# Performance work log

Measured on AMD Instinct MI355X. Metric: run time of the kernel, lower is better.

The kernel has to match this reference:

```python
import jax, jax.numpy as jnp
import numpy as np

WL = 140        # window_length
TD_NUM = 14     # TimeDelayEnd - TimeDelaySta = 21 - 7
OFC = 119       # window_length - TimeDelayEnd
E1 = 119        # td_attn embed dim
E2 = 16         # cm_attn embed dim


def _mha(q, k, v, in_w, in_b, out_w, out_b):
    # single-head MultiheadAttention, torch convention: y = x @ W.T + b
    E = q.shape[-1]
    qp = q @ in_w[:E].T + in_b[:E]
    kp = k @ in_w[E:2 * E].T + in_b[E:2 * E]
    vp = v @ in_w[2 * E:].T + in_b[2 * E:]
    attn = jax.nn.softmax((qp * (E ** -0.5)) @ kp.T, axis=-1)
    return (attn @ vp) @ out_w.T + out_b


def setup_inputs() -> dict:
    key = jax.random.key(0)
    ks = jax.random.split(key, 24)
    n = lambda i, s: jax.random.normal(ks[i], s, dtype=jnp.float32) * 0.05
    return {
        "x": jax.random.normal(ks[0], (1, 1, 18, WL), dtype=jnp.float32),
        "td_in_w": n(1, (3 * E1, E1)), "td_in_b": n(2, (3 * E1,)),
        "td_out_w": n(3, (E1, E1)), "td_out_b": n(4, (E1,)),
        "cm_in_w": n(5, (4, 3 * E2, E2)), "cm_in_b": n(6, (4, 3 * E2)),
        "cm_out_w": n(7, (4, E2, E2)), "cm_out_b": n(8, (4, E2)),
        "mc_w": n(9, (2, 16)), "mc_b": n(10, (2,)),
        "max_fc_w": n(11, (16, 32)), "max_fc_b": n(12, (16,)),
        "proj_w": n(13, (2, 16)),
        "ln_g": jnp.ones((16,), jnp.float32), "ln_b": jnp.zeros((16,), jnp.float32),
        "fc_w": n(14, (2,)), "fc_b": n(15, (2,)),
        "out1_w": n(16, (OFC, 2 * OFC)), "out1_b": n(17, (OFC,)),
        "out2_w": n(18, (2, OFC)), "out2_b": n(19, (2,)),
    }


def reference(x, td_in_w, td_in_b, td_out_w, td_out_b,
              cm_in_w, cm_in_b, cm_out_w, cm_out_b,
              mc_w, mc_b, max_fc_w, max_fc_b, proj_w,
              ln_g, ln_b, fc_w, fc_b, out1_w, out1_b, out2_w, out2_b):
    wavA = x[0, 0, 0]            # [140]
    eeg = x[0, 0, 1:17]          # [16, 140]
    wavB = x[0, 0, 17]           # [140]

    # ChannelWav: vectorized sliding-window gather -> [OFC, TD_NUM]
    idx = jnp.arange(OFC)[:, None] + jnp.arange(TD_NUM)[None, :]
    wA_win = wavA[idx]           # [119, 14]
    wB_win = wavB[idx]

    eeg_q = eeg[:, WL - OFC:]    # [16, 119] (16 eeg channels as seq, embed=119)

    # time-delay attention: query=eeg (len 16), key/value=delayed wav (len 14)
    wA_att = _mha(eeg_q, wA_win.T, wA_win.T, td_in_w, td_in_b, td_out_w, td_out_b)  # [16,119]
    wB_att = _mha(eeg_q, wB_win.T, wB_win.T, td_in_w, td_in_b, td_out_w, td_out_b)

    # select_max: bmm + 1x1 conv + relu + fc + argmax over 16 scores
    vA = jax.nn.relu(mc_w[0] @ (eeg_q @ wA_att.T) + mc_b[0])   # [16]
    vB = jax.nn.relu(mc_w[1] @ (eeg_q @ wB_att.T) + mc_b[1])
    weight = jax.nn.relu(max_fc_w @ jnp.concatenate([vA, vB]) + max_fc_b)
    mi = jnp.argmax(weight)     # note: clamped into [0, TD_NUM) by jnp.take
    wA_sel = jnp.take(wA_win.T, mi, axis=0)   # [119]
    wB_sel = jnp.take(wB_win.T, mi, axis=0)

    # proj_audio: Conv1d(1,16,1,bias=False) == outer product with weight vector
    wA_p = proj_w[0][:, None] * wA_sel[None, :]   # [16,119]
    wB_p = proj_w[1][:, None] * wB_sel[None, :]

    # LayerNorm over the 16-channel axis
    et = eeg_q.T                                   # [119,16]
    mu = et.mean(-1, keepdims=True)
    var = et.var(-1, keepdims=True)
    eeg_ln = (((et - mu) / jnp.sqrt(var + 1e-5)) * ln_g + ln_b).T   # [16,119]

    data = [wA_p, eeg_ln, eeg_ln, wB_p]
    kv = [eeg_ln, wA_p, wB_p, eeg_ln]
    outs = [_mha(data[i].T, kv[i].T, kv[i].T,
                 cm_in_w[i], cm_in_b[i], cm_out_w[i], cm_out_b[i]).T
            for i in range(4)]                      # each [16,119]

    # tensordot + diag == per-position channel dot product
    d0 = jnp.einsum('ct,ct->t', outs[0], outs[1])   # [119]
    d1 = jnp.einsum('ct,ct->t', outs[3], outs[2])
    s0 = jax.nn.sigmoid(fc_w[0] * d0 + fc_b[0])
    s1 = jax.nn.sigmoid(fc_w[1] * d1 + fc_b[1])
    dd = jnp.concatenate([s0, s1])                  # [238]

    h = jax.nn.sigmoid(out1_w @ dd + out1_b)
    return jax.nn.sigmoid(out2_w @ h + out2_b)[None, :]   # [1,2]
```

## Files before the change

### kernel.cpp

```cpp
#include <hip/hip_runtime.h>
#include <math.h>


#define NWG 8
#define NT  1024

constexpr int WLEN = 140;
constexpr int TDN  = 14;
constexpr int NOFC = 119;

constexpr int G_V16 = 0;
constexpr int G_DD  = 64;

constexpr int EEG = 0;
constexpr int WA  = 1904;
constexpr int WB  = 2044;
constexpr int LNT = 2184;
constexpr int QP4 = 4088;
constexpr int Z4  = 4564;
constexpr int UD  = 5040;
constexpr int WTT = 5160;
constexpr int WVV = 5280;
constexpr int VT  = 5400;
constexpr int SC4 = 5416;
constexpr int BKQ = 5472;
constexpr int CVB = 5476, CBO = 5477;
constexpr int WQH = 5480;
constexpr int WKL = 5496;
constexpr int WVL = 5512;
constexpr int WQT = 5528;
constexpr int CST = 5544;
constexpr int AC  = 5548;
constexpr int BC  = 5564;
constexpr int G1L = 5580;
constexpr int MXT = 5612;
constexpr int MXB = 6124;
constexpr int WK2 = 6852;
constexpr int C2K = 6868;
constexpr int CQK = 6884;
constexpr int CBK = 6885;
constexpr int VPS = 8756;
constexpr int S1H = 11136;
constexpr int S2H = 11255;
constexpr int OWS = 11376;
constexpr int OBS = 11632;
constexpr int O1W = 11648;
constexpr int O1B = 15248;
constexpr int O2WS= 15264;
constexpr int O2B = 15294;
constexpr int FCW = 15296;
constexpr int FCB = 15298;
constexpr int DDL = 15300;
constexpr int HHL = 15538;
constexpr int VSL = 15554;
constexpr int ARENA = 15586;

struct Args {
  const float *x, *td_in_w, *td_in_b, *td_out_w, *td_out_b;
  const float *cm_in_w, *cm_in_b, *cm_out_w, *cm_out_b;
  const float *mc_w, *mc_b, *max_fc_w, *max_fc_b, *proj_w;
  const float *ln_g, *ln_b, *fc_w, *fc_b;
  const float *out1_w, *out1_b, *out2_w, *out2_b;
  float *out;
  unsigned int *bar;
  float *G;
};

__device__ __forceinline__ float sigmf(float v) {
  return 1.0f / (1.0f + __expf(-v));
}

__device__ __forceinline__ void gbar(unsigned int* p) {
  __syncthreads();
  if (threadIdx.x == 0) {
    __hip_atomic_fetch_add(p, 1u, __ATOMIC_ACQ_REL, __HIP_MEMORY_SCOPE_AGENT);
    while (__hip_atomic_load(p, __ATOMIC_RELAXED, __HIP_MEMORY_SCOPE_AGENT) < (unsigned)NWG) {
      __builtin_amdgcn_s_sleep(1);
    }
    __builtin_amdgcn_fence(__ATOMIC_ACQUIRE, "agent");
  }
  __syncthreads();
}

__device__ __forceinline__ float dot119(const float* __restrict__ w,
                                        const float* __restrict__ x,
                                        int lane16) {
  float a0 = 0.f, a1 = 0.f;
#pragma unroll
  for (int t = 0; t < 7; ++t) {
    float wv = w[lane16 + 16 * t];
    float xv = x[lane16 + 16 * t];
    if (t & 1) a1 += wv * xv; else a0 += wv * xv;
  }
  if (lane16 < 7) a0 += w[112 + lane16] * x[112 + lane16];
  float acc = a0 + a1;
#pragma unroll
  for (int m = 1; m < 16; m <<= 1) acc += __shfl_xor(acc, m);
  return acc;
}

__device__ __forceinline__ float dot16f4(const float* __restrict__ x,
                                         const float* __restrict__ w) {
  const float4* xa = (const float4*)x; const float4* wa = (const float4*)w;
  float4 x0 = xa[0], x1 = xa[1], x2 = xa[2], x3 = xa[3];
  float4 w0 = wa[0], w1 = wa[1], w2 = wa[2], w3 = wa[3];
  float d0 = x0.x*w0.x + x0.y*w0.y + x0.z*w0.z + x0.w*w0.w;
  float d1 = x1.x*w1.x + x1.y*w1.y + x1.z*w1.z + x1.w*w1.w;
  float d2 = x2.x*w2.x + x2.y*w2.y + x2.z*w2.z + x2.w*w2.w;
  float d3 = x3.x*w3.x + x3.y*w3.y + x3.z*w3.z + x3.w*w3.w;
  return (d0 + d1) + (d2 + d3);
}

__global__ __launch_bounds__(NT) void fused_cnn_kernel(Args a) {
  __shared__ __align__(16) float S[ARENA];
  const int tid = threadIdx.x;
  const int wgid = blockIdx.x;
  const int grp = tid >> 4;
  const int lane16 = tid & 15;
  float* G = a.G;

  const int s  = wgid >> 2;
  const int i0 = (wgid & 3) * 4;
  const int mh = s ? 3 : 0;
  const int lm = s ? 2 : 1;
  const int q4 = wgid & 3;
  const int r0 = q4 * 30;
  const int nr = (q4 == 3) ? 29 : 30;
  const int wavX = s ? WB : WA;

  for (int t = tid; t < 16 * NOFC; t += NT) {
    int c = t / NOFC, tt = t - c * NOFC;
    S[EEG + t] = a.x[(1 + c) * WLEN + (WLEN - NOFC) + tt];
  }
  if (tid < WLEN) {
    S[WA + tid] = a.x[tid];
    S[WB + tid] = a.x[17 * WLEN + tid];
  }
  if (tid < 512) {
    int t16 = tid >> 5, c32 = tid & 31;
    S[MXT + c32 * 16 + t16] = a.max_fc_w[tid];
  }
  if (tid < 16)  S[MXB + tid] = a.max_fc_b[tid];
  if (tid < 256) {
    int c = tid >> 4, e = tid & 15;
    S[OWS + e * 16 + c] = a.cm_out_w[mh * 256 + tid];
  }
  if (tid < 16)  S[OBS + tid] = a.cm_out_b[mh * 16 + tid];
  for (int idx = tid; idx < 15 * 238; idx += NT) {
    int rl = idx / 238, c = idx - rl * 238;
    int r = wgid * 15 + rl;
    S[O1W + rl * 240 + c] = (r < NOFC) ? a.out1_w[r * 238 + c] : 0.0f;
  }
  if (tid < 15) {
    int r = wgid * 15 + tid;
    S[O1B + tid] = (r < NOFC) ? a.out1_b[r] : 0.0f;
  }
  if (tid < 30) {
    int o = tid / 15, j = tid - o * 15;
    int r = wgid * 15 + j;
    S[O2WS + tid] = (r < NOFC) ? a.out2_w[o * NOFC + r] : 0.0f;
  }
  if (tid < 2) {
    S[O2B + tid] = a.out2_b[tid];
    S[FCW + tid] = a.fc_w[tid];
    S[FCB + tid] = a.fc_b[tid];
  }
  __syncthreads();

  for (int e = grp; e < NOFC; e += 64) {
    const float* wrow = a.td_in_w + e * NOFC;
    float w0 = wrow[lane16], w1 = wrow[lane16 + 16], w2 = wrow[lane16 + 32],
          w3 = wrow[lane16 + 48], w4 = wrow[lane16 + 64], w5 = wrow[lane16 + 80],
          w6 = wrow[lane16 + 96];
    float wt7 = (lane16 < 7) ? wrow[112 + lane16] : 0.0f;
    float b = a.td_in_b[e];
#pragma unroll
    for (int kk = 0; kk < 4; ++kk) {
      const float* x = S + EEG + (i0 + kk) * NOFC;
      float acc = w0 * x[lane16] + w1 * x[lane16 + 16] + w2 * x[lane16 + 32]
                + w3 * x[lane16 + 48] + w4 * x[lane16 + 64] + w5 * x[lane16 + 80]
                + w6 * x[lane16 + 96];
      if (lane16 < 7) acc += wt7 * x[112 + lane16];
#pragma unroll
      for (int mm = 1; mm < 16; mm <<= 1) acc += __shfl_xor(acc, mm);
      if (lane16 == 0) S[QP4 + kk * NOFC + e] = acc + b;
    }
  }
  if (grp >= 55) {
    int d = (grp - 55) * 16 + lane16;
    if (d < NOFC) {
      float acc = 0.f;
#pragma unroll
      for (int i = 0; i < 16; ++i) acc += a.mc_w[s * 16 + i] * S[EEG + i * NOFC + d];
      S[UD + d] = acc;
    }
  }
  __syncthreads();

  if (tid < NOFC) {
    float a0 = 0.f, a1 = 0.f, a2 = 0.f, a3 = 0.f;
    const float* base = a.td_in_w + NOFC * NOFC + tid;
    for (int e = 0; e < NOFC; ++e) {
      float w = base[e * NOFC];
      a0 += S[QP4 + e] * w;
      a1 += S[QP4 + NOFC + e] * w;
      a2 += S[QP4 + 2 * NOFC + e] * w;
      a3 += S[QP4 + 3 * NOFC + e] * w;
    }
    S[Z4 + tid] = a0; S[Z4 + NOFC + tid] = a1;
    S[Z4 + 2 * NOFC + tid] = a2; S[Z4 + 3 * NOFC + tid] = a3;
  } else if (tid >= 128 && tid < 128 + NOFC) {
    int t = tid - 128;
    float acc = 0.f;
    const float* base = a.td_out_w + t;
    for (int d = 0; d < NOFC; ++d) acc += S[UD + d] * base[d * NOFC];
    S[WTT + t] = acc;
  } else if (tid >= 256 && tid < 256 + NOFC) {
    int t = tid - 256;
    float xv[16]; float mu = 0.f;
#pragma unroll
    for (int c = 0; c < 16; ++c) { xv[c] = S[EEG + c * NOFC + t]; mu += xv[c]; }
    mu *= (1.0f / 16.0f);
    float var = 0.f;
#pragma unroll
    for (int c = 0; c < 16; ++c) { float d = xv[c] - mu; var += d * d; }
    var *= (1.0f / 16.0f);
    float inv = 1.0f / sqrtf(var + 1e-5f);
#pragma unroll
    for (int c = 0; c < 16; ++c)
      S[LNT + t * 16 + c] = (xv[c] - mu) * inv * a.ln_g[c] + a.ln_b[c];
  } else if (tid >= 384 && tid < 448) {
    int kk = (tid - 384) >> 4;
    float acc = dot119(S + QP4 + kk * NOFC, a.td_in_b + NOFC, lane16);
    if (lane16 == 0) S[BKQ + kk] = acc;
  } else if (tid >= 448 && tid < 464) {
    int e = tid - 448;
    float acc = 0.f;
#pragma unroll
    for (int c = 0; c < 16; ++c) acc += a.proj_w[s * 16 + c] * a.cm_in_w[(mh * 48 + e) * 16 + c];
    S[WQH + e] = acc;
  } else if (tid >= 464 && tid < 480) {
    int e = tid - 464;
    float acc = 0.f;
#pragma unroll
    for (int c = 0; c < 16; ++c) acc += a.proj_w[s * 16 + c] * a.cm_in_w[(lm * 48 + 16 + e) * 16 + c];
    S[WKL + e] = acc;
  } else if (tid >= 480 && tid < 496) {
    int e = tid - 480;
    float acc = 0.f;
#pragma unroll
    for (int c = 0; c < 16; ++c) acc += a.proj_w[s * 16 + c] * a.cm_in_w[(lm * 48 + 32 + e) * 16 + c];
    S[WVL + e] = acc;
  }
  __syncthreads();

  if (tid < NOFC) {
    float acc = 0.f;
    const float* base = a.td_in_w + 2 * NOFC * NOFC + tid;
    for (int e = 0; e < NOFC; ++e) acc += S[WTT + e] * base[e * NOFC];
    S[WVV + tid] = acc;
  } else if (tid == 124) {
    float acc = 0.f;
#pragma unroll
    for (int e = 0; e < 16; ++e) acc += S[WQH + e] * a.cm_in_b[mh * 48 + 16 + e];
    S[CQK] = acc;
  } else if (tid == 125) {
    float acc = 0.f;
#pragma unroll
    for (int e = 0; e < 16; ++e) acc += a.cm_in_b[mh * 48 + e] * a.cm_in_b[mh * 48 + 16 + e];
    S[CBK] = acc;
  } else if (tid >= 128 && tid < 144) {
    int c = tid - 128;
    float acc = 0.f;
#pragma unroll
    for (int e = 0; e < 16; ++e) acc += S[WQH + e] * a.cm_in_w[(mh * 48 + 16 + e) * 16 + c];
    S[WK2 + c] = acc;
  } else if (tid >= 144 && tid < 160) {
    int c = tid - 144;
    float acc = 0.f;
#pragma unroll
    for (int e = 0; e < 16; ++e) acc += a.cm_in_b[mh * 48 + e] * a.cm_in_w[(mh * 48 + 16 + e) * 16 + c];
    S[C2K + c] = acc;
  } else if (tid >= 160 && tid < 592) {
    for (int o = tid - 160; o < 1904; o += 432) {
      int u = o >> 4, e = o & 15;
      S[VPS + u * 20 + e] = dot16f4(S + LNT + u * 16, a.cm_in_w + (mh * 48 + 32 + e) * 16)
                            + a.cm_in_b[mh * 48 + 32 + e];
    }
  }
  if (grp >= 37) {
#pragma unroll
    for (int rnd = 0; rnd < 3; ++rnd) {
      int idx = (grp - 37) + rnd * 27;
      if (idx < 56) {
        int kk = idx / TDN, j = idx - kk * TDN;
        float acc = dot119(S + wavX + j, S + Z4 + kk * NOFC, lane16);
        if (lane16 == 0)
          S[SC4 + kk * TDN + j] = 0.09166984970282113f * (acc + S[BKQ + kk]);
      }
    }
  }
  __syncthreads();

  if (grp < TDN) {
    float acc = dot119(S + wavX + grp, S + WVV, lane16);
    if (lane16 == 0) S[VT + grp] = acc;
  } else if (tid >= 224 && tid < 228) {
    int k = tid - 224;
    float* r = S + SC4 + k * TDN;
    float mx = r[0];
#pragma unroll
    for (int j = 1; j < TDN; ++j) mx = fmaxf(mx, r[j]);
    float sum = 0.f;
#pragma unroll
    for (int j = 0; j < TDN; ++j) { float p = __expf(r[j] - mx); r[j] = p; sum += p; }
    float inv = 1.0f / sum;
#pragma unroll
    for (int j = 0; j < TDN; ++j) r[j] *= inv;
  } else if (grp == 15) {
    float acc = dot119(a.td_in_b + 2 * NOFC, S + WTT, lane16);
    if (lane16 == 0) S[CVB] = acc;
  } else if (grp == 16) {
    float acc = dot119(S + UD, a.td_out_b, lane16);
    if (lane16 == 0) S[CBO] = acc;
  } else if (tid >= 288 && tid < 304) {
    int c = tid - 288;
    float acc = 0.f;
#pragma unroll
    for (int e = 0; e < 16; ++e) acc += a.cm_in_w[(lm * 48 + e) * 16 + c] * S[WKL + e];
    S[WQT + c] = acc;
  } else if (tid == 304) {
    float acc = 0.f;
#pragma unroll
    for (int e = 0; e < 16; ++e) acc += a.cm_in_b[lm * 48 + e] * S[WKL + e];
    S[CST] = acc;
  } else if (tid >= 320 && tid < 336) {
    int c = tid - 320;
    float acc = 0.f;
#pragma unroll
    for (int e = 0; e < 16; ++e) acc += a.cm_out_w[lm * 256 + c * 16 + e] * S[WVL + e];
    S[AC + c] = acc;
  } else if (tid >= 336 && tid < 352) {
    int c = tid - 336;
    float acc = 0.f;
#pragma unroll
    for (int e = 0; e < 16; ++e) acc += a.cm_out_w[lm * 256 + c * 16 + e] * a.cm_in_b[lm * 48 + 32 + e];
    S[BC + c] = acc + a.cm_out_b[lm * 16 + c];
  }
  if (tid >= 512 && tid < 750) {
    int idx = tid - 512;
    int u = (idx < NOFC) ? idx : idx - NOFC;
    const float* lr = S + LNT + u * 16;
    float acc = 0.f;
    if (idx < NOFC) {
#pragma unroll
      for (int c = 0; c < 16; ++c) acc += S[WK2 + c] * lr[c];
      S[S1H + u] = acc + S[CQK];
    } else {
#pragma unroll
      for (int c = 0; c < 16; ++c) acc += S[C2K + c] * lr[c];
      S[S2H + u] = acc + S[CBK];
    }
  }
  __syncthreads();

  if (tid < 4) {
    float acc = 0.f;
#pragma unroll
    for (int j = 0; j < TDN; ++j) acc += S[SC4 + tid * TDN + j] * S[VT + j];
    float v = acc + S[CVB] + S[CBO] + a.mc_b[s];
    G[G_V16 + s * 16 + i0 + tid] = fmaxf(v, 0.f);
  } else if (tid >= 32 && tid < 62) {
    int rl = tid - 32;
    if (rl < nr) {
      int t = r0 + rl;
      float acc = S[CST];
#pragma unroll
      for (int c = 0; c < 16; ++c) acc += S[LNT + t * 16 + c] * S[WQT + c];
      S[G1L + rl] = acc;
    }
  }
  gbar(a.bar + 0);

  if (tid < 32) S[VSL + tid] = G[G_V16 + tid];
  __syncthreads();
  int mi;
  {
    float wl = S[MXB + lane16];
#pragma unroll
    for (int c = 0; c < 32; ++c) wl += S[MXT + c * 16 + lane16] * S[VSL + c];
    wl = fmaxf(wl, 0.f);
    float mx = wl;
#pragma unroll
    for (int d = 1; d < 16; d <<= 1) mx = fmaxf(mx, __shfl_xor(mx, d));
    int cand = (wl == mx) ? lane16 : 99;
#pragma unroll
    for (int d = 1; d < 16; d <<= 1) cand = min(cand, __shfl_xor(cand, d));
    mi = min(cand, TDN - 1);
  }

  if (grp < nr) {
    const int t = r0 + grp;
    const float wselq = S[wavX + t + mi];
    float p[8];
    float sum = 0.f;
#pragma unroll
    for (int cc = 0; cc < 8; ++cc) {
      int u = lane16 + cc * 16;
      float e1 = 0.f;
      if (u < NOFC)
        e1 = __expf(0.25f * (wselq * S[S1H + u] + S[S2H + u]));
      p[cc] = e1;
      sum += e1;
    }
#pragma unroll
    for (int d = 1; d < 16; d <<= 1) sum += __shfl_xor(sum, d);
    float inv = 1.0f / sum;

    float oa[16];
#pragma unroll
    for (int e = 0; e < 16; ++e) oa[e] = 0.f;
#pragma unroll
    for (int cc = 0; cc < 8; ++cc) {
      int u = lane16 + cc * 16;
      if (u < NOFC) {
        const float4* v4 = (const float4*)(S + VPS + u * 20);
        float4 v0 = v4[0], v1 = v4[1], v2 = v4[2], v3 = v4[3];
        float pv = p[cc];
        oa[0] += pv*v0.x; oa[1] += pv*v0.y; oa[2] += pv*v0.z; oa[3] += pv*v0.w;
        oa[4] += pv*v1.x; oa[5] += pv*v1.y; oa[6] += pv*v1.z; oa[7] += pv*v1.w;
        oa[8] += pv*v2.x; oa[9] += pv*v2.y; oa[10] += pv*v2.z; oa[11] += pv*v2.w;
        oa[12] += pv*v3.x; oa[13] += pv*v3.y; oa[14] += pv*v3.z; oa[15] += pv*v3.w;
      }
    }
#pragma unroll
    for (int e = 0; e < 16; ++e) {
#pragma unroll
      for (int d = 1; d < 16; d <<= 1) oa[e] += __shfl_xor(oa[e], d);
    }
    float oc = S[OBS + lane16];
#pragma unroll
    for (int e = 0; e < 16; ++e) oc += oa[e] * inv * S[OWS + e * 16 + lane16];
    float dA = oc * S[AC + lane16];
    float dB = oc * S[BC + lane16];
#pragma unroll
    for (int d = 1; d < 16; d <<= 1) {
      dA += __shfl_xor(dA, d);
      dB += __shfl_xor(dB, d);
    }
    const float g = S[G1L + grp];
    float s0 = 0.f, s1a = 0.f;
#pragma unroll
    for (int cc = 0; cc < 8; ++cc) {
      int u = lane16 + cc * 16;
      if (u < NOFC) {
        float w = S[wavX + u + mi];
        float e1 = __expf(0.25f * g * w);
        s0 += e1; s1a += e1 * w;
      }
    }
#pragma unroll
    for (int d = 1; d < 16; d <<= 1) {
      s0 += __shfl_xor(s0, d);
      s1a += __shfl_xor(s1a, d);
    }
    float h = s1a / s0;
    float dval = h * dA + dB;
    if (lane16 == 0)
      G[G_DD + s * NOFC + t] = sigmf(S[FCW + s] * dval + S[FCB + s]);
  }
  gbar(a.bar + 16);

  if (tid < 238) S[DDL + tid] = G[G_DD + tid];
  __syncthreads();
  if (grp < 15) {
    int r = wgid * 15 + grp;
    float acc = 0.f;
#pragma unroll
    for (int k = 0; k < 15; ++k) {
      int c = lane16 + 16 * k;
      if (c < 238) acc += S[O1W + grp * 240 + c] * S[DDL + c];
    }
#pragma unroll
    for (int d = 1; d < 16; d <<= 1) acc += __shfl_xor(acc, d);
    if (lane16 == 0)
      S[HHL + grp] = (r < NOFC) ? sigmf(acc + S[O1B + grp]) : 0.0f;
  }
  __syncthreads();
  if (tid == 0) {
    float p0 = 0.f, p1 = 0.f;
#pragma unroll
    for (int j = 0; j < 15; ++j) {
      p0 += S[O2WS + j] * S[HHL + j];
      p1 += S[O2WS + 15 + j] * S[HHL + j];
    }
    float* acc = (float*)((char*)a.bar + 128);
    unsigned int* done = (unsigned int*)((char*)a.bar + 192);
    __hip_atomic_fetch_add(acc + 0, p0, __ATOMIC_RELAXED, __HIP_MEMORY_SCOPE_AGENT);
    __hip_atomic_fetch_add(acc + 1, p1, __ATOMIC_RELAXED, __HIP_MEMORY_SCOPE_AGENT);
    unsigned old = __hip_atomic_fetch_add(done, 1u, __ATOMIC_ACQ_REL, __HIP_MEMORY_SCOPE_AGENT);
    if (old == NWG - 1) {
      __builtin_amdgcn_fence(__ATOMIC_ACQUIRE, "agent");
      float a0 = __hip_atomic_load(acc + 0, __ATOMIC_RELAXED, __HIP_MEMORY_SCOPE_AGENT);
      float a1 = __hip_atomic_load(acc + 1, __ATOMIC_RELAXED, __HIP_MEMORY_SCOPE_AGENT);
      a.out[0] = sigmf(a0 + S[O2B + 0]);
      a.out[1] = sigmf(a1 + S[O2B + 1]);
    }
  }
}

extern "C" void kernel_launch(void* const* d_in, const int* in_sizes, int n_in,
                              void* d_out, int out_size, void* d_ws, size_t ws_size,
                              hipStream_t stream) {
  Args a;
  a.x        = (const float*)d_in[0];
  a.td_in_w  = (const float*)d_in[1];
  a.td_in_b  = (const float*)d_in[2];
  a.td_out_w = (const float*)d_in[3];
  a.td_out_b = (const float*)d_in[4];
  a.cm_in_w  = (const float*)d_in[5];
  a.cm_in_b  = (const float*)d_in[6];
  a.cm_out_w = (const float*)d_in[7];
  a.cm_out_b = (const float*)d_in[8];
  a.mc_w     = (const float*)d_in[9];
  a.mc_b     = (const float*)d_in[10];
  a.max_fc_w = (const float*)d_in[11];
  a.max_fc_b = (const float*)d_in[12];
  a.proj_w   = (const float*)d_in[13];
  a.ln_g     = (const float*)d_in[14];
  a.ln_b     = (const float*)d_in[15];
  a.fc_w     = (const float*)d_in[16];
  a.fc_b     = (const float*)d_in[17];
  a.out1_w   = (const float*)d_in[18];
  a.out1_b   = (const float*)d_in[19];
  a.out2_w   = (const float*)d_in[20];
  a.out2_b   = (const float*)d_in[21];
  a.out      = (float*)d_out;
  a.bar      = (unsigned int*)d_ws;
  a.G        = (float*)((char*)d_ws + 512);

  hipMemsetAsync(d_ws, 0, 512, stream);
  fused_cnn_kernel<<<dim3(NWG), dim3(NT), 0, stream>>>(a);
}
```

Baseline: 33.53 us.

## Rebalance phase work to shorten dependency chain and drop LDS staging barriers

Computes the mc_w projection of EEG directly from global x in the load phase. This lets the td_out_w matvec run alongside the Q projection, and the V-chain matvecs and small cross-modal precomputations each move one phase earlier. Softmax over the 14 delays is fused with the weighted sum, which removes a separate normalise pass and one __syncthreads phase. After each grid barrier, values are read straight from global G instead of being staged into LDS with an extra __syncthreads. The risks are repeated global reads per thread and fewer thread groups for the Q projection.

Result: faster. 31.56 us (-5.9%).

```diff
diff --git a/kernel.cpp b/kernel.cpp
--- a/kernel.cpp
+++ b/kernel.cpp
@@ -50,10 +50,8 @@
 constexpr int O2B = 15294;
 constexpr int FCW = 15296;
 constexpr int FCB = 15298;
-constexpr int DDL = 15300;
-constexpr int HHL = 15538;
-constexpr int VSL = 15554;
-constexpr int ARENA = 15586;
+constexpr int HHL = 15300;
+constexpr int ARENA = 15316;
 
 struct Args {
   const float *x, *td_in_w, *td_in_b, *td_out_w, *td_out_b;
@@ -165,35 +163,42 @@
     S[FCW + tid] = a.fc_w[tid];
     S[FCB + tid] = a.fc_b[tid];
   }
-  __syncthreads();
-
-  for (int e = grp; e < NOFC; e += 64) {
-    const float* wrow = a.td_in_w + e * NOFC;
-    float w0 = wrow[lane16], w1 = wrow[lane16 + 16], w2 = wrow[lane16 + 32],
-          w3 = wrow[lane16 + 48], w4 = wrow[lane16 + 64], w5 = wrow[lane16 + 80],
-          w6 = wrow[lane16 + 96];
-    float wt7 = (lane16 < 7) ? wrow[112 + lane16] : 0.0f;
-    float b = a.td_in_b[e];
-#pragma unroll
-    for (int kk = 0; kk < 4; ++kk) {
-      const float* x = S + EEG + (i0 + kk) * NOFC;
-      float acc = w0 * x[lane16] + w1 * x[lane16 + 16] + w2 * x[lane16 + 32]
-                + w3 * x[lane16 + 48] + w4 * x[lane16 + 64] + w5 * x[lane16 + 80]
-                + w6 * x[lane16 + 96];
-      if (lane16 < 7) acc += wt7 * x[112 + lane16];
-#pragma unroll
-      for (int mm = 1; mm < 16; mm <<= 1) acc += __shfl_xor(acc, mm);
-      if (lane16 == 0) S[QP4 + kk * NOFC + e] = acc + b;
-    }
-  }
-  if (grp >= 55) {
-    int d = (grp - 55) * 16 + lane16;
-    if (d < NOFC) {
-      float acc = 0.f;
-#pragma unroll
-      for (int i = 0; i < 16; ++i) acc += a.mc_w[s * 16 + i] * S[EEG + i * NOFC + d];
-      S[UD + d] = acc;
-    }
+  if (tid >= 896 && tid < 896 + NOFC) {
+    int d = tid - 896;
+    float acc = 0.f;
+#pragma unroll
+    for (int i = 0; i < 16; ++i)
+      acc += a.mc_w[s * 16 + i] * a.x[(1 + i) * WLEN + (WLEN - NOFC) + d];
+    S[UD + d] = acc;
+  }
+  __syncthreads();
+
+  if (grp < 48) {
+    for (int e = grp; e < NOFC; e += 48) {
+      const float* wrow = a.td_in_w + e * NOFC;
+      float w0 = wrow[lane16], w1 = wrow[lane16 + 16], w2 = wrow[lane16 + 32],
+            w3 = wrow[lane16 + 48], w4 = wrow[lane16 + 64], w5 = wrow[lane16 + 80],
+            w6 = wrow[lane16 + 96];
+      float wt7 = (lane16 < 7) ? wrow[112 + lane16] : 0.0f;
+      float b = a.td_in_b[e];
+#pragma unroll
+      for (int kk = 0; kk < 4; ++kk) {
+        const float* x = S + EEG + (i0 + kk) * NOFC;
+        float acc = w0 * x[lane16] + w1 * x[lane16 + 16] + w2 * x[lane16 + 32]
+                  + w3 * x[lane16 + 48] + w4 * x[lane16 + 64] + w5 * x[lane16 + 80]
+                  + w6 * x[lane16 + 96];
+        if (lane16 < 7) acc += wt7 * x[112 + lane16];
+#pragma unroll
+        for (int mm = 1; mm < 16; mm <<= 1) acc += __shfl_xor(acc, mm);
+        if (lane16 == 0) S[QP4 + kk * NOFC + e] = acc + b;
+      }
+    }
+  } else if (tid >= 768 && tid < 768 + NOFC) {
+    int t = tid - 768;
+    float acc = 0.f;
+    const float* base = a.td_out_w + t;
+    for (int d = 0; d < NOFC; ++d) acc += S[UD + d] * base[d * NOFC];
+    S[WTT + t] = acc;
   }
   __syncthreads();
 
@@ -211,12 +216,6 @@
     S[Z4 + 2 * NOFC + tid] = a2; S[Z4 + 3 * NOFC + tid] = a3;
   } else if (tid >= 128 && tid < 128 + NOFC) {
     int t = tid - 128;
-    float acc = 0.f;
-    const float* base = a.td_out_w + t;
-    for (int d = 0; d < NOFC; ++d) acc += S[UD + d] * base[d * NOFC];
-    S[WTT + t] = acc;
-  } else if (tid >= 256 && tid < 256 + NOFC) {
-    int t = tid - 256;
     float xv[16]; float mu = 0.f;
 #pragma unroll
     for (int c = 0; c < 16; ++c) { xv[c] = S[EEG + c * NOFC + t]; mu += xv[c]; }
@@ -229,6 +228,12 @@
 #pragma unroll
     for (int c = 0; c < 16; ++c)
       S[LNT + t * 16 + c] = (xv[c] - mu) * inv * a.ln_g[c] + a.ln_b[c];
+  } else if (tid >= 256 && tid < 256 + NOFC) {
+    int t = tid - 256;
+    float acc = 0.f;
+    const float* base = a.td_in_w + 2 * NOFC * NOFC + t;
+    for (int e = 0; e < NOFC; ++e) acc += S[WTT + e] * base[e * NOFC];
+    S[WVV + t] = acc;
   } else if (tid >= 384 && tid < 448) {
     int kk = (tid - 384) >> 4;
     float acc = dot119(S + QP4 + kk * NOFC, a.td_in_b + NOFC, lane16);
@@ -254,44 +259,71 @@
   }
   __syncthreads();
 
-  if (tid < NOFC) {
-    float acc = 0.f;
-    const float* base = a.td_in_w + 2 * NOFC * NOFC + tid;
-    for (int e = 0; e < NOFC; ++e) acc += S[WTT + e] * base[e * NOFC];
-    S[WVV + tid] = acc;
-  } else if (tid == 124) {
+  if (grp < TDN) {
+    float acc = dot119(S + wavX + grp, S + WVV, lane16);
+    if (lane16 == 0) S[VT + grp] = acc;
+  } else if (grp == 14) {
+    float acc = dot119(a.td_in_b + 2 * NOFC, S + WTT, lane16);
+    if (lane16 == 0) S[CVB] = acc;
+  } else if (grp == 15) {
+    float acc = dot119(S + UD, a.td_out_b, lane16);
+    if (lane16 == 0) S[CBO] = acc;
+  } else if (tid >= 256 && tid < 272) {
+    int c = tid - 256;
+    float acc = 0.f;
+#pragma unroll
+    for (int e = 0; e < 16; ++e) acc += S[WQH + e] * a.cm_in_w[(mh * 48 + 16 + e) * 16 + c];
+    S[WK2 + c] = acc;
+  } else if (tid >= 272 && tid < 288) {
+    int c = tid - 272;
+    float acc = 0.f;
+#pragma unroll
+    for (int e = 0; e < 16; ++e) acc += a.cm_in_b[mh * 48 + e] * a.cm_in_w[(mh * 48 + 16 + e) * 16 + c];
+    S[C2K + c] = acc;
+  } else if (tid == 288) {
     float acc = 0.f;
 #pragma unroll
     for (int e = 0; e < 16; ++e) acc += S[WQH + e] * a.cm_in_b[mh * 48 + 16 + e];
     S[CQK] = acc;
-  } else if (tid == 125) {
+  } else if (tid == 289) {
     float acc = 0.f;
 #pragma unroll
     for (int e = 0; e < 16; ++e) acc += a.cm_in_b[mh * 48 + e] * a.cm_in_b[mh * 48 + 16 + e];
     S[CBK] = acc;
-  } else if (tid >= 128 && tid < 144) {
-    int c = tid - 128;
-    float acc = 0.f;
-#pragma unroll
-    for (int e = 0; e < 16; ++e) acc += S[WQH + e] * a.cm_in_w[(mh * 48 + 16 + e) * 16 + c];
-    S[WK2 + c] = acc;
-  } else if (tid >= 144 && tid < 160) {
-    int c = tid - 144;
-    float acc = 0.f;
-#pragma unroll
-    for (int e = 0; e < 16; ++e) acc += a.cm_in_b[mh * 48 + e] * a.cm_in_w[(mh * 48 + 16 + e) * 16 + c];
-    S[C2K + c] = acc;
-  } else if (tid >= 160 && tid < 592) {
-    for (int o = tid - 160; o < 1904; o += 432) {
+  } else if (tid >= 304 && tid < 320) {
+    int c = tid - 304;
+    float acc = 0.f;
+#pragma unroll
+    for (int e = 0; e < 16; ++e) acc += a.cm_in_w[(lm * 48 + e) * 16 + c] * S[WKL + e];
+    S[WQT + c] = acc;
+  } else if (tid == 320) {
+    float acc = 0.f;
+#pragma unroll
+    for (int e = 0; e < 16; ++e) acc += a.cm_in_b[lm * 48 + e] * S[WKL + e];
+    S[CST] = acc;
+  } else if (tid >= 336 && tid < 352) {
+    int c = tid - 336;
+    float acc = 0.f;
+#pragma unroll
+    for (int e = 0; e < 16; ++e) acc += a.cm_out_w[lm * 256 + c * 16 + e] * S[WVL + e];
+    S[AC + c] = acc;
+  } else if (tid >= 352 && tid < 368) {
+    int c = tid - 352;
+    float acc = 0.f;
+#pragma unroll
+    for (int e = 0; e < 16; ++e) acc += a.cm_out_w[lm * 256 + c * 16 + e] * a.cm_in_b[lm * 48 + 32 + e];
+    S[BC + c] = acc + a.cm_out_b[lm * 16 + c];
+  } else if (tid >= 368 && tid < 640) {
+    for (int o = tid - 368; o < 1904; o += 272) {
       int u = o >> 4, e = o & 15;
       S[VPS + u * 20 + e] = dot16f4(S + LNT + u * 16, a.cm_in_w + (mh * 48 + 32 + e) * 16)
                             + a.cm_in_b[mh * 48 + 32 + e];
     }
   }
-  if (grp >= 37) {
+  if (grp >= 40) {
 #pragma unroll
     for (int rnd = 0; rnd < 3; ++rnd) {
-      int idx = (grp - 37) + rnd * 27;
+      int idx = (grp - 40) + rnd * 24;
       if (idx < 56) {
         int kk = idx / TDN, j = idx - kk * TDN;
         float acc = dot119(S + wavX + j, S + Z4 + kk * NOFC, lane16);
@@ -302,73 +334,19 @@
   }
   __syncthreads();
 
-  if (grp < TDN) {
-    float acc = dot119(S + wavX + grp, S + WVV, lane16);
-    if (lane16 == 0) S[VT + grp] = acc;
-  } else if (tid >= 224 && tid < 228) {
-    int k = tid - 224;
-    float* r = S + SC4 + k * TDN;
+  if (tid < 4) {
+    const float* r = S + SC4 + tid * TDN;
     float mx = r[0];
 #pragma unroll
     for (int j = 1; j < TDN; ++j) mx = fmaxf(mx, r[j]);
-    float sum = 0.f;
-#pragma unroll
-    for (int j = 0; j < TDN; ++j) { float p = __expf(r[j] - mx); r[j] = p; sum += p; }
-    float inv = 1.0f / sum;
-#pragma unroll
-    for (int j = 0; j < TDN; ++j) r[j] *= inv;
-  } else if (grp == 15) {
-    float acc = dot119(a.td_in_b + 2 * NOFC, S + WTT, lane16);
-    if (lane16 == 0) S[CVB] = acc;
-  } else if (grp == 16) {
-    float acc = dot119(S + UD, a.td_out_b, lane16);
-    if (lane16 == 0) S[CBO] = acc;
-  } else if (tid >= 288 && tid < 304) {
-    int c = tid - 288;
-    float acc = 0.f;
-#pragma unroll
-    for (int e = 0; e < 16; ++e) acc += a.cm_in_w[(lm * 48 + e) * 16 + c] * S[WKL + e];
-    S[WQT + c] = acc;
-  } else if (tid == 304) {
-    float acc = 0.f;
-#pragma unroll
-    for (int e = 0; e < 16; ++e) acc += a.cm_in_b[lm * 48 + e] * S[WKL + e];
-    S[CST] = acc;
-  } else if (tid >= 320 && tid < 336) {
-    int c = tid - 320;
-    float acc = 0.f;
-#pragma unroll
-    for (int e = 0; e < 16; ++e) acc += a.cm_out_w[lm * 256 + c * 16 + e] * S[WVL + e];
-    S[AC + c] = acc;
-  } else if (tid >= 336 && tid < 352) {
-    int c = tid - 336;
-    float acc = 0.f;
-#pragma unroll
-    for (int e = 0; e < 16; ++e) acc += a.cm_out_w[lm * 256 + c * 16 + e] * a.cm_in_b[lm * 48 + 32 + e];
-    S[BC + c] = acc + a.cm_out_b[lm * 16 + c];
-  }
-  if (tid >= 512 && tid < 750) {
-    int idx = tid - 512;
-    int u = (idx < NOFC) ? idx : idx - NOFC;
-    const float* lr = S + LNT + u * 16;
-    float acc = 0.f;
-    if (idx < NOFC) {
-#pragma unroll
-      for (int c = 0; c < 16; ++c) acc += S[WK2 + c] * lr[c];
-      S[S1H + u] = acc + S[CQK];
-    } else {
-#pragma unroll
-      for (int c = 0; c < 16; ++c) acc += S[C2K + c] * lr[c];
-      S[S2H + u] = acc + S[CBK];
-    }
-  }
-  __syncthreads();
-
-  if (tid < 4) {
-    float acc = 0.f;
-#pragma unroll
-    for (int j = 0; j < TDN; ++j) acc += S[SC4 + tid * TDN + j] * S[VT + j];
-    float v = acc + S[CVB] + S[CBO] + a.mc_b[s];
+    float sum = 0.f, acc = 0.f;
+#pragma unroll
+    for (int j = 0; j < TDN; ++j) {
+      float p = __expf(r[j] - mx);
+      sum += p;
+      acc += p * S[VT + j];
+    }
+    float v = acc / sum + S[CVB] + S[CBO] + a.mc_b[s];
     G[G_V16 + s * 16 + i0 + tid] = fmaxf(v, 0.f);
   } else if (tid >= 32 && tid < 62) {
     int rl = tid - 32;
@@ -380,15 +358,28 @@
       S[G1L + rl] = acc;
     }
   }
+  if (tid >= 512 && tid < 750) {
+    int idx = tid - 512;
+    int u = (idx < NOFC) ? idx : idx - NOFC;
+    const float* lr = S + LNT + u * 16;
+    float acc = 0.f;
+    if (idx < NOFC) {
+#pragma unroll
+      for (int c = 0; c < 16; ++c) acc += S[WK2 + c] * lr[c];
+      S[S1H + u] = acc + S[CQK];
+    } else {
+#pragma unroll
+      for (int c = 0; c < 16; ++c) acc += S[C2K + c] * lr[c];
+      S[S2H + u] = acc + S[CBK];
+    }
+  }
   gbar(a.bar + 0);
 
-  if (tid < 32) S[VSL + tid] = G[G_V16 + tid];
-  __syncthreads();
   int mi;
   {
     float wl = S[MXB + lane16];
 #pragma unroll
-    for (int c = 0; c < 32; ++c) wl += S[MXT + c * 16 + lane16] * S[VSL + c];
+    for (int c = 0; c < 32; ++c) wl += S[MXT + c * 16 + lane16] * G[G_V16 + c];
     wl = fmaxf(wl, 0.f);
     float mx = wl;
 #pragma unroll
@@ -471,15 +462,13 @@
   }
   gbar(a.bar + 16);
 
-  if (tid < 238) S[DDL + tid] = G[G_DD + tid];
-  __syncthreads();
   if (grp < 15) {
     int r = wgid * 15 + grp;
     float acc = 0.f;
 #pragma unroll
     for (int k = 0; k < 15; ++k) {
       int c = lane16 + 16 * k;
-      if (c < 238) acc += S[O1W + grp * 240 + c] * S[DDL + c];
+      if (c < 238) acc += S[O1W + grp * 240 + c] * G[G_DD + c];
     }
 #pragma unroll
     for (int d = 1; d < 16; d <<= 1) acc += __shfl_xor(acc, d);
```
